# Optimization experiments

Measured on AMD Instinct MI355X. Metric: run time of the kernel, lower is better.

Reference implementation:

```python
import jax, jax.numpy as jnp
import numpy as np
from jax import lax

B, T, P, H, O = 64, 96, 256, 128, 24  # batch, seq_len, num_points, hidden_dim, pred_len


def setup_inputs() -> dict:
    key = jax.random.key(0)
    ks = jax.random.split(key, 7)
    s = 1.0 / np.sqrt(H)  # torch LSTM/Linear default init scale
    return {
        "x": jax.random.normal(ks[0], (B, T, P, 1), dtype=jnp.float32),
        "W_ih": jax.random.uniform(ks[1], (P, 4 * H, 1), jnp.float32, -s, s),
        "W_hh": jax.random.uniform(ks[2], (P, 4 * H, H), jnp.float32, -s, s),
        "b_ih": jax.random.uniform(ks[3], (P, 4 * H), jnp.float32, -s, s),
        "b_hh": jax.random.uniform(ks[4], (P, 4 * H), jnp.float32, -s, s),
        "W_fc": jax.random.uniform(ks[5], (P, O, H), jnp.float32, -s, s),
        "b_fc": jax.random.uniform(ks[6], (P, O), jnp.float32, -s, s),
    }


def reference(x, W_ih, W_hh, b_ih, b_hh, W_fc, b_fc):
    # x: [B, T, P, F]; model uses only feature 0
    xs = x[..., 0]  # [B, T, P]
    # input_dim == 1, so input-to-gate contribution is a scaled broadcast of W_ih
    # precompute for all timesteps: [T, B, P, 4H]
    gx = jnp.einsum("btp,pg->tbpg", xs, W_ih[:, :, 0]) + (b_ih + b_hh)

    def step(carry, gxt):
        h, c = carry  # [B, P, H] each
        gates = gxt + jnp.einsum("bph,pgh->bpg", h, W_hh)  # [B, P, 4H]
        i, f, g, o = jnp.split(gates, 4, axis=-1)  # torch gate order i,f,g,o
        i = jax.nn.sigmoid(i)
        f = jax.nn.sigmoid(f)
        g = jnp.tanh(g)
        o = jax.nn.sigmoid(o)
        c = f * c + i * g
        h = o * jnp.tanh(c)
        return (h, c), None

    h0 = jnp.zeros((B, P, H), dtype=x.dtype)
    (h, _), _ = lax.scan(step, (h0, h0), gx)
    # per-point Linear on final hidden state: [B, P, O]
    out = jnp.einsum("bph,poh->bpo", h, W_fc) + b_fc
    # original stacks point outputs on last dim -> [B, pred_len, P]
    return jnp.transpose(out, (0, 2, 1))
```

## Files before the change

### kernel.cpp

```cpp
#include <hip/hip_runtime.h>
#include <hip/hip_bf16.h>

#define Bdim 64
#define Tdim 96
#define Pdim 256
#define Hdim 128
#define Gdim 512
#define Odim 24
#define BH   32

typedef _Float16 f16x8 __attribute__((ext_vector_type(8)));
typedef float    f32x16 __attribute__((ext_vector_type(16)));
typedef float    f32x2  __attribute__((ext_vector_type(2)));

union H8 { uint4 u4; unsigned short s[8]; _Float16 h[8]; f16x8 v; };
union HS { _Float16 h; unsigned short s; };

__device__ __forceinline__ float exp2_fast(float x) {
#if __has_builtin(__builtin_amdgcn_exp2f)
    return __builtin_amdgcn_exp2f(x);
#else
    return __expf(x * 0.6931471805599453f);
#endif
}

__global__ __launch_bounds__(1024, 4)
void lstm_fused(const float* __restrict__ x,
                const float* __restrict__ W_ih,
                const float* __restrict__ W_hh,
                const float* __restrict__ b_ih,
                const float* __restrict__ b_hh,
                const float* __restrict__ W_fc,
                const float* __restrict__ b_fc,
                float* __restrict__ out)
{
    __shared__ unsigned short hb0[2][BH * Hdim];
    __shared__ unsigned short hb1[2][BH * Hdim];

    const int p   = blockIdx.x;
    const int tid = threadIdx.x;
    const int w   = tid >> 6;
    const int l31 = tid & 31;
    const int hi  = (tid >> 5) & 1;

    const float L1 = 1.4426950408889634f;
    const float L2 = 2.0f * L1;

    for (int i = tid; i < 2 * BH * Hdim; i += 1024) ((unsigned short*)hb0)[i] = 0;
    for (int i = tid; i < 2 * BH * Hdim; i += 1024) ((unsigned short*)hb1)[i] = 0;

    f16x8 afr[9];
    {
        const int rp   = w * 32 + l31;
        const int orow = ((rp & 3) << 7) | (rp >> 2);
        const float sc = ((rp & 3) == 2) ? L2 : L1;
        const float* rowp = W_hh + (size_t)p * Gdim * Hdim + (size_t)orow * Hdim;
        #pragma unroll
        for (int ks = 0; ks < 8; ++ks) {
            int k0 = ks * 16 + hi * 8;
            float4 va = *(const float4*)(rowp + k0);
            float4 vb = *(const float4*)(rowp + k0 + 4);
            H8 u;
            u.h[0] = (_Float16)(sc * va.x); u.h[1] = (_Float16)(sc * va.y);
            u.h[2] = (_Float16)(sc * va.z); u.h[3] = (_Float16)(sc * va.w);
            u.h[4] = (_Float16)(sc * vb.x); u.h[5] = (_Float16)(sc * vb.y);
            u.h[6] = (_Float16)(sc * vb.z); u.h[7] = (_Float16)(sc * vb.w);
            afr[ks] = u.v;
        }
        H8 u9;
        #pragma unroll
        for (int j = 0; j < 8; ++j) u9.s[j] = 0;
        if (hi == 0) {
            u9.h[0] = (_Float16)(sc * W_ih[(size_t)p * Gdim + orow]);
            u9.h[1] = (_Float16)(sc * (b_ih[(size_t)p * Gdim + orow] +
                                       b_hh[(size_t)p * Gdim + orow]));
        }
        afr[8] = u9.v;
    }

    auto ldh = [&](const unsigned short* hb, int ks) -> H8 {
        H8 r;
        int c   = ks * 2 + hi;
        int off = (l31 << 8) + ((c ^ (l31 & 15)) << 4);
        r.u4 = *(const uint4*)((const char*)hb + off);
        return r;
    };

    auto ep_pair = [&](const f32x16& a, int j, f32x2* cr, unsigned short* wb) {
        f32x2 yi = {a[8 * j + 0], a[8 * j + 4]};
        f32x2 yf = {a[8 * j + 1], a[8 * j + 5]};
        f32x2 yg = {a[8 * j + 2], a[8 * j + 6]};
        f32x2 yo = {a[8 * j + 3], a[8 * j + 7]};
        f32x2 Ef = {exp2_fast(-yf.x), exp2_fast(-yf.y)};
        f32x2 Ei = {exp2_fast(-yi.x), exp2_fast(-yi.y)};
        f32x2 Eg = {exp2_fast(yg.x),  exp2_fast(yg.y)};
        f32x2 t1 = Ef + 1.0f;
        f32x2 t2 = Ei + 1.0f;
        f32x2 t3 = Eg + 1.0f;
        f32x2 t4 = Eg - 1.0f;
        f32x2 den = (t1 * t2) * t3;
        f32x2 num = (cr[j] * t2) * t3 + (L2 * t4) * t1;
        float D = den.x * den.y;
        float r = __builtin_amdgcn_rcpf(D);
        f32x2 inv = {r * den.y, r * den.x};
        f32x2 cn  = num * inv;
        cn.x = __builtin_amdgcn_fmed3f(cn.x, -30.0f, 30.0f);
        cn.y = __builtin_amdgcn_fmed3f(cn.y, -30.0f, 30.0f);
        cr[j] = cn;
        f32x2 Eo = {exp2_fast(-yo.x), exp2_fast(-yo.y)};
        f32x2 Ec = {exp2_fast(cn.x),  exp2_fast(cn.y)};
        f32x2 d2 = (Eo + 1.0f) * (Ec + 1.0f);
        float D2 = d2.x * d2.y;
        float r2 = __builtin_amdgcn_rcpf(D2);
        f32x2 j2 = {r2 * d2.y, r2 * d2.x};
        f32x2 hv = (Ec - 1.0f) * j2;
        HS ha; ha.h = (_Float16)hv.x;
        HS hc; hc.h = (_Float16)hv.y;
        int base = (l31 << 7) + ((w ^ (l31 & 15)) << 3) + 4 * j + hi;
        wb[base]     = ha.s;
        wb[base + 2] = hc.s;
    };

    auto phase = [&](const unsigned short* rb, unsigned short* wb,
                     f32x16& acc, const f32x16& ar, f32x2* cr, float xv,
                     bool doGemm, bool doEp) {
        if (doGemm) {
            H8 f0 = ldh(rb, 0), f1 = ldh(rb, 1);
            H8 f2 = ldh(rb, 2), f3 = ldh(rb, 3);
            f32x16 z;
            #pragma unroll
            for (int j = 0; j < 16; ++j) z[j] = 0.f;
            acc = __builtin_amdgcn_mfma_f32_32x32x16_f16(afr[0], f0.v, z, 0, 0, 0);
            acc = __builtin_amdgcn_mfma_f32_32x32x16_f16(afr[1], f1.v, acc, 0, 0, 0);
            if (doEp) ep_pair(ar, 0, cr, wb);
            H8 f4 = ldh(rb, 4), f5 = ldh(rb, 5);
            acc = __builtin_amdgcn_mfma_f32_32x32x16_f16(afr[2], f2.v, acc, 0, 0, 0);
            acc = __builtin_amdgcn_mfma_f32_32x32x16_f16(afr[3], f3.v, acc, 0, 0, 0);
            if (doEp) ep_pair(ar, 1, cr, wb);
            H8 f6 = ldh(rb, 6), f7 = ldh(rb, 7);
            acc = __builtin_amdgcn_mfma_f32_32x32x16_f16(afr[4], f4.v, acc, 0, 0, 0);
            acc = __builtin_amdgcn_mfma_f32_32x32x16_f16(afr[5], f5.v, acc, 0, 0, 0);
            acc = __builtin_amdgcn_mfma_f32_32x32x16_f16(afr[6], f6.v, acc, 0, 0, 0);
            acc = __builtin_amdgcn_mfma_f32_32x32x16_f16(afr[7], f7.v, acc, 0, 0, 0);
            H8 bg;
            #pragma unroll
            for (int j = 0; j < 8; ++j) bg.s[j] = 0;
            if (hi == 0) { bg.h[0] = (_Float16)xv; bg.h[1] = (_Float16)1.0f; }
            acc = __builtin_amdgcn_mfma_f32_32x32x16_f16(afr[8], bg.v, acc, 0, 0, 0);
        } else if (doEp) {
            ep_pair(ar, 0, cr, wb);
            ep_pair(ar, 1, cr, wb);
        }
    };

    f32x2 cre0[2] = {f32x2{0.f, 0.f}, f32x2{0.f, 0.f}};
    f32x2 cre1[2] = {f32x2{0.f, 0.f}, f32x2{0.f, 0.f}};
    f32x16 acc0, acc1;
    #pragma unroll
    for (int j = 0; j < 16; ++j) { acc0[j] = 0.f; acc1[j] = 0.f; }

    const float* xp0 = x + (size_t)((0 * BH + l31) * Tdim) * Pdim + p;
    const float* xp1 = x + (size_t)((1 * BH + l31) * Tdim) * Pdim + p;
    float xv1 = xp1[0];

    __syncthreads();

    {
        float xv0 = xp0[0];
        phase(hb0[0], hb1[0], acc0, acc1, cre1, xv0, true, false);
    }
    __syncthreads();

    for (int t = 0; t < Tdim; ++t) {
        const int P  = t & 1;
        const int tn = (t + 1 < Tdim) ? (t + 1) : t;
        float xn0 = xp0[(size_t)tn * Pdim];

        phase(hb1[P], hb0[P ^ 1], acc1, acc0, cre0, xv1, true, true);
        __syncthreads();

        float xn1 = xp1[(size_t)tn * Pdim];
        if (t + 1 < Tdim) {
            phase(hb0[P ^ 1], hb1[P ^ 1], acc0, acc1, cre1, xn0, true, true);
        } else {
            phase(hb0[P ^ 1], hb1[P ^ 1], acc0, acc1, cre1, 0.f, false, true);
        }
        __syncthreads();
        xv1 = xn1;
    }

    const float* wfc = W_fc + (size_t)p * Odim * Hdim;
    const float* bfc = b_fc + (size_t)p * Odim;
    for (int i = tid; i < Bdim * Odim; i += 1024) {
        int o = i % Odim;
        int b = i / Odim;
        int bl = (b < BH) ? b : (b - BH);
        const unsigned short* hr = (b < BH) ? (hb0[0] + (bl << 7))
                                            : (hb1[0] + (bl << 7));
        float s = bfc[o];
        const float* wr = wfc + o * Hdim;
        #pragma unroll 8
        for (int k2 = 0; k2 < Hdim; ++k2) {
            int idx = (((k2 >> 3) ^ (bl & 15)) << 3) + (k2 & 7);
            HS s2; s2.s = hr[idx];
            s = __builtin_fmaf(wr[k2], (float)s2.h, s);
        }
        out[(size_t)b * Odim * Pdim + (size_t)o * Pdim + p] = s;
    }
}

extern "C" void kernel_launch(void* const* d_in, const int* in_sizes, int n_in,
                              void* d_out, int out_size, void* d_ws, size_t ws_size,
                              hipStream_t stream) {
    const float* x    = (const float*)d_in[0];
    const float* W_ih = (const float*)d_in[1];
    const float* W_hh = (const float*)d_in[2];
    const float* b_ih = (const float*)d_in[3];
    const float* b_hh = (const float*)d_in[4];
    const float* W_fc = (const float*)d_in[5];
    const float* b_fc = (const float*)d_in[6];
    float* out = (float*)d_out;

    lstm_fused<<<dim3(Pdim), dim3(1024), 0, stream>>>(x, W_ih, W_hh, b_ih, b_hh, W_fc, b_fc, out);
}
```

Before: 390.9 us.

## Split batch halves across separate blocks, each wave computing two gate tiles

Each point now gets two 512-thread blocks, one per batch half of 32, where before one 1024-thread block interleaved both halves in a software-pipelined ping-pong. Each wave holds two M-tiles of W_hh (16 fragments) and issues two interleaved MFMA chains that share the same h fragments. The bias/input term moves into a packed register, and hidden-state writes become packed 8-byte stores. This removes the two-phase interleaving and one barrier per step, and doubles the block count to fill more CUs, at the cost of loading W_hh twice per point and more VGPRs per thread.

```diff
diff --git a/kernel.cpp b/kernel.cpp
--- a/kernel.cpp
+++ b/kernel.cpp
@@ -9,12 +9,14 @@
 #define Odim 24
 #define BH   32
 
-typedef _Float16 f16x8 __attribute__((ext_vector_type(8)));
+typedef _Float16 f16x8  __attribute__((ext_vector_type(8)));
+typedef __fp16   fp16x2 __attribute__((ext_vector_type(2)));
 typedef float    f32x16 __attribute__((ext_vector_type(16)));
 typedef float    f32x2  __attribute__((ext_vector_type(2)));
 
-union H8 { uint4 u4; unsigned short s[8]; _Float16 h[8]; f16x8 v; };
+union H8 { uint4 u4; unsigned int u[4]; unsigned short s[8]; _Float16 h[8]; f16x8 v; };
 union HS { _Float16 h; unsigned short s; };
+union PK2 { fp16x2 v; unsigned int u; };
 
 __device__ __forceinline__ float exp2_fast(float x) {
 #if __has_builtin(__builtin_amdgcn_exp2f)
@@ -24,7 +26,9 @@
 #endif
 }
 
-__global__ __launch_bounds__(1024, 4)
+#define MFMA __builtin_amdgcn_mfma_f32_32x32x16_f16
+
+__global__ __launch_bounds__(512, 4)
 void lstm_fused(const float* __restrict__ x,
                 const float* __restrict__ W_ih,
                 const float* __restrict__ W_hh,
@@ -34,178 +38,169 @@
                 const float* __restrict__ b_fc,
                 float* __restrict__ out)
 {
-    __shared__ unsigned short hb0[2][BH * Hdim];
-    __shared__ unsigned short hb1[2][BH * Hdim];
-
-    const int p   = blockIdx.x;
-    const int tid = threadIdx.x;
-    const int w   = tid >> 6;
-    const int l31 = tid & 31;
-    const int hi  = (tid >> 5) & 1;
+    __shared__ unsigned short hbuf[2][BH * Hdim];
+
+    const int p    = blockIdx.x >> 1;
+    const int half = blockIdx.x & 1;
+    const int tid  = threadIdx.x;
+    const int w    = tid >> 6;
+    const int l31  = tid & 31;
+    const int hi   = (tid >> 5) & 1;
 
     const float L1 = 1.4426950408889634f;
     const float L2 = 2.0f * L1;
 
-    for (int i = tid; i < 2 * BH * Hdim; i += 1024) ((unsigned short*)hb0)[i] = 0;
-    for (int i = tid; i < 2 * BH * Hdim; i += 1024) ((unsigned short*)hb1)[i] = 0;
-
-    f16x8 afr[9];
+    for (int i = tid; i < 2 * BH * Hdim; i += 512) ((unsigned short*)hbuf)[i] = 0;
+
+    f16x8 afr[2][8];
+    unsigned int gxp[2];
     {
-        const int rp   = w * 32 + l31;
-        const int orow = ((rp & 3) << 7) | (rp >> 2);
-        const float sc = ((rp & 3) == 2) ? L2 : L1;
-        const float* rowp = W_hh + (size_t)p * Gdim * Hdim + (size_t)orow * Hdim;
+        const int gate = l31 & 3;
+        const float sc = (gate == 2) ? L2 : L1;
         #pragma unroll
-        for (int ks = 0; ks < 8; ++ks) {
-            int k0 = ks * 16 + hi * 8;
-            float4 va = *(const float4*)(rowp + k0);
-            float4 vb = *(const float4*)(rowp + k0 + 4);
-            H8 u;
-            u.h[0] = (_Float16)(sc * va.x); u.h[1] = (_Float16)(sc * va.y);
-            u.h[2] = (_Float16)(sc * va.z); u.h[3] = (_Float16)(sc * va.w);
-            u.h[4] = (_Float16)(sc * vb.x); u.h[5] = (_Float16)(sc * vb.y);
-            u.h[6] = (_Float16)(sc * vb.z); u.h[7] = (_Float16)(sc * vb.w);
-            afr[ks] = u.v;
-        }
-        H8 u9;
-        #pragma unroll
-        for (int j = 0; j < 8; ++j) u9.s[j] = 0;
-        if (hi == 0) {
-            u9.h[0] = (_Float16)(sc * W_ih[(size_t)p * Gdim + orow]);
-            u9.h[1] = (_Float16)(sc * (b_ih[(size_t)p * Gdim + orow] +
-                                       b_hh[(size_t)p * Gdim + orow]));
-        }
-        afr[8] = u9.v;
+        for (int m = 0; m < 2; ++m) {
+            const int kk   = 16 * w + 8 * m + 4 * ((l31 >> 2) & 1) + (l31 >> 3);
+            const int orow = gate * 128 + kk;
+            const float* rowp = W_hh + (size_t)p * Gdim * Hdim + (size_t)orow * Hdim;
+            #pragma unroll
+            for (int ks = 0; ks < 8; ++ks) {
+                int k0 = ks * 16 + hi * 8;
+                float4 va = *(const float4*)(rowp + k0);
+                float4 vb = *(const float4*)(rowp + k0 + 4);
+                H8 u;
+                u.h[0] = (_Float16)(sc * va.x); u.h[1] = (_Float16)(sc * va.y);
+                u.h[2] = (_Float16)(sc * va.z); u.h[3] = (_Float16)(sc * va.w);
+                u.h[4] = (_Float16)(sc * vb.x); u.h[5] = (_Float16)(sc * vb.y);
+                u.h[6] = (_Float16)(sc * vb.z); u.h[7] = (_Float16)(sc * vb.w);
+                afr[m][ks] = u.v;
+            }
+            HS ga, gb;
+            ga.h = (_Float16)(sc * W_ih[(size_t)p * Gdim + orow]);
+            gb.h = (_Float16)(sc * (b_ih[(size_t)p * Gdim + orow] +
+                                    b_hh[(size_t)p * Gdim + orow]));
+            gxp[m] = hi ? 0u : ((unsigned int)ga.s | ((unsigned int)gb.s << 16));
+        }
     }
 
-    auto ldh = [&](const unsigned short* hb, int ks) -> H8 {
-        H8 r;
-        int c   = ks * 2 + hi;
-        int off = (l31 << 8) + ((c ^ (l31 & 15)) << 4);
-        r.u4 = *(const uint4*)((const char*)hb + off);
-        return r;
-    };
-
-    auto ep_pair = [&](const f32x16& a, int j, f32x2* cr, unsigned short* wb) {
-        f32x2 yi = {a[8 * j + 0], a[8 * j + 4]};
-        f32x2 yf = {a[8 * j + 1], a[8 * j + 5]};
-        f32x2 yg = {a[8 * j + 2], a[8 * j + 6]};
-        f32x2 yo = {a[8 * j + 3], a[8 * j + 7]};
-        f32x2 Ef = {exp2_fast(-yf.x), exp2_fast(-yf.y)};
-        f32x2 Ei = {exp2_fast(-yi.x), exp2_fast(-yi.y)};
-        f32x2 Eg = {exp2_fast(yg.x),  exp2_fast(yg.y)};
-        f32x2 t1 = Ef + 1.0f;
-        f32x2 t2 = Ei + 1.0f;
-        f32x2 t3 = Eg + 1.0f;
-        f32x2 t4 = Eg - 1.0f;
-        f32x2 den = (t1 * t2) * t3;
-        f32x2 num = (cr[j] * t2) * t3 + (L2 * t4) * t1;
-        float D = den.x * den.y;
-        float r = __builtin_amdgcn_rcpf(D);
-        f32x2 inv = {r * den.y, r * den.x};
-        f32x2 cn  = num * inv;
-        cn.x = __builtin_amdgcn_fmed3f(cn.x, -30.0f, 30.0f);
-        cn.y = __builtin_amdgcn_fmed3f(cn.y, -30.0f, 30.0f);
-        cr[j] = cn;
-        f32x2 Eo = {exp2_fast(-yo.x), exp2_fast(-yo.y)};
-        f32x2 Ec = {exp2_fast(cn.x),  exp2_fast(cn.y)};
-        f32x2 d2 = (Eo + 1.0f) * (Ec + 1.0f);
-        float D2 = d2.x * d2.y;
-        float r2 = __builtin_amdgcn_rcpf(D2);
-        f32x2 j2 = {r2 * d2.y, r2 * d2.x};
-        f32x2 hv = (Ec - 1.0f) * j2;
-        HS ha; ha.h = (_Float16)hv.x;
-        HS hc; hc.h = (_Float16)hv.y;
-        int base = (l31 << 7) + ((w ^ (l31 & 15)) << 3) + 4 * j + hi;
-        wb[base]     = ha.s;
-        wb[base + 2] = hc.s;
-    };
-
-    auto phase = [&](const unsigned short* rb, unsigned short* wb,
-                     f32x16& acc, const f32x16& ar, f32x2* cr, float xv,
-                     bool doGemm, bool doEp) {
-        if (doGemm) {
-            H8 f0 = ldh(rb, 0), f1 = ldh(rb, 1);
-            H8 f2 = ldh(rb, 2), f3 = ldh(rb, 3);
+    const int rb0 = (l31 << 8) | ((hi ^ (l31 & 15)) << 4);
+    const int wo0 = (l31 << 8) + (((2 * w + 0) ^ (l31 & 15)) << 4) + (hi << 3);
+    const int wo1 = (l31 << 8) + (((2 * w + 1) ^ (l31 & 15)) << 4) + (hi << 3);
+
+    f32x2 cre[4];
+    #pragma unroll
+    for (int i = 0; i < 4; ++i) cre[i] = f32x2{0.f, 0.f};
+
+    const float* xp = x + (size_t)((half * BH + l31) * Tdim) * Pdim + p;
+    float xv = xp[0];
+
+    __syncthreads();
+
+    for (int t = 0; t < Tdim; ++t) {
+        const unsigned short* rbuf = hbuf[t & 1];
+        unsigned short* wbuf = hbuf[(t & 1) ^ 1];
+        const char* rc = (const char*)rbuf;
+        float xn = xp[(size_t)((t + 1 < Tdim) ? t + 1 : t) * Pdim];
+
+        PK2 xb; xb.v = __builtin_amdgcn_cvt_pkrtz(xv, 1.0f);
+        H8 bg; bg.u[0] = hi ? 0u : xb.u; bg.u[1] = 0; bg.u[2] = 0; bg.u[3] = 0;
+        H8 g0; g0.u[0] = gxp[0]; g0.u[1] = 0; g0.u[2] = 0; g0.u[3] = 0;
+        H8 g1; g1.u[0] = gxp[1]; g1.u[1] = 0; g1.u[2] = 0; g1.u[3] = 0;
+
+        f32x16 acc0, acc1;
+        {
+            H8 f0, f1, f2, f3, f4, f5, f6, f7;
+            f0.u4 = *(const uint4*)(rc + (rb0 ^ (0 << 5)));
+            f1.u4 = *(const uint4*)(rc + (rb0 ^ (1 << 5)));
+            f2.u4 = *(const uint4*)(rc + (rb0 ^ (2 << 5)));
+            f3.u4 = *(const uint4*)(rc + (rb0 ^ (3 << 5)));
             f32x16 z;
             #pragma unroll
             for (int j = 0; j < 16; ++j) z[j] = 0.f;
-            acc = __builtin_amdgcn_mfma_f32_32x32x16_f16(afr[0], f0.v, z, 0, 0, 0);
-            acc = __builtin_amdgcn_mfma_f32_32x32x16_f16(afr[1], f1.v, acc, 0, 0, 0);
-            if (doEp) ep_pair(ar, 0, cr, wb);
-            H8 f4 = ldh(rb, 4), f5 = ldh(rb, 5);
-            acc = __builtin_amdgcn_mfma_f32_32x32x16_f16(afr[2], f2.v, acc, 0, 0, 0);
-            acc = __builtin_amdgcn_mfma_f32_32x32x16_f16(afr[3], f3.v, acc, 0, 0, 0);
-            if (doEp) ep_pair(ar, 1, cr, wb);
-            H8 f6 = ldh(rb, 6), f7 = ldh(rb, 7);
-            acc = __builtin_amdgcn_mfma_f32_32x32x16_f16(afr[4], f4.v, acc, 0, 0, 0);
-            acc = __builtin_amdgcn_mfma_f32_32x32x16_f16(afr[5], f5.v, acc, 0, 0, 0);
-            acc = __builtin_amdgcn_mfma_f32_32x32x16_f16(afr[6], f6.v, acc, 0, 0, 0);
-            acc = __builtin_amdgcn_mfma_f32_32x32x16_f16(afr[7], f7.v, acc, 0, 0, 0);
-            H8 bg;
+            acc0 = MFMA(afr[0][0], f0.v, z, 0, 0, 0);
+            acc1 = MFMA(afr[1][0], f0.v, z, 0, 0, 0);
+            f4.u4 = *(const uint4*)(rc + (rb0 ^ (4 << 5)));
+            acc0 = MFMA(afr[0][1], f1.v, acc0, 0, 0, 0);
+            acc1 = MFMA(afr[1][1], f1.v, acc1, 0, 0, 0);
+            f5.u4 = *(const uint4*)(rc + (rb0 ^ (5 << 5)));
+            acc0 = MFMA(afr[0][2], f2.v, acc0, 0, 0, 0);
+            acc1 = MFMA(afr[1][2], f2.v, acc1, 0, 0, 0);
+            f6.u4 = *(const uint4*)(rc + (rb0 ^ (6 << 5)));
+            acc0 = MFMA(afr[0][3], f3.v, acc0, 0, 0, 0);
+            acc1 = MFMA(afr[1][3], f3.v, acc1, 0, 0, 0);
+            f7.u4 = *(const uint4*)(rc + (rb0 ^ (7 << 5)));
+            acc0 = MFMA(afr[0][4], f4.v, acc0, 0, 0, 0);
+            acc1 = MFMA(afr[1][4], f4.v, acc1, 0, 0, 0);
+            acc0 = MFMA(afr[0][5], f5.v, acc0, 0, 0, 0);
+            acc1 = MFMA(afr[1][5], f5.v, acc1, 0, 0, 0);
+            acc0 = MFMA(afr[0][6], f6.v, acc0, 0, 0, 0);
+            acc1 = MFMA(afr[1][6], f6.v, acc1, 0, 0, 0);
+            acc0 = MFMA(afr[0][7], f7.v, acc0, 0, 0, 0);
+            acc1 = MFMA(afr[1][7], f7.v, acc1, 0, 0, 0);
+            acc0 = MFMA(g0.v, bg.v, acc0, 0, 0, 0);
+            acc1 = MFMA(g1.v, bg.v, acc1, 0, 0, 0);
+        }
+
+        #pragma unroll
+        for (int m = 0; m < 2; ++m) {
+            const f32x16& a = m ? acc1 : acc0;
+            f32x2 hv[2];
             #pragma unroll
-            for (int j = 0; j < 8; ++j) bg.s[j] = 0;
-            if (hi == 0) { bg.h[0] = (_Float16)xv; bg.h[1] = (_Float16)1.0f; }
-            acc = __builtin_amdgcn_mfma_f32_32x32x16_f16(afr[8], bg.v, acc, 0, 0, 0);
-        } else if (doEp) {
-            ep_pair(ar, 0, cr, wb);
-            ep_pair(ar, 1, cr, wb);
-        }
-    };
-
-    f32x2 cre0[2] = {f32x2{0.f, 0.f}, f32x2{0.f, 0.f}};
-    f32x2 cre1[2] = {f32x2{0.f, 0.f}, f32x2{0.f, 0.f}};
-    f32x16 acc0, acc1;
-    #pragma unroll
-    for (int j = 0; j < 16; ++j) { acc0[j] = 0.f; acc1[j] = 0.f; }
-
-    const float* xp0 = x + (size_t)((0 * BH + l31) * Tdim) * Pdim + p;
-    const float* xp1 = x + (size_t)((1 * BH + l31) * Tdim) * Pdim + p;
-    float xv1 = xp1[0];
-
-    __syncthreads();
-
-    {
-        float xv0 = xp0[0];
-        phase(hb0[0], hb1[0], acc0, acc1, cre1, xv0, true, false);
-    }
-    __syncthreads();
-
-    for (int t = 0; t < Tdim; ++t) {
-        const int P  = t & 1;
-        const int tn = (t + 1 < Tdim) ? (t + 1) : t;
-        float xn0 = xp0[(size_t)tn * Pdim];
-
-        phase(hb1[P], hb0[P ^ 1], acc1, acc0, cre0, xv1, true, true);
+            for (int j = 0; j < 2; ++j) {
+                f32x2 yi = {a[8 * j + 0], a[8 * j + 4]};
+                f32x2 yf = {a[8 * j + 1], a[8 * j + 5]};
+                f32x2 yg = {a[8 * j + 2], a[8 * j + 6]};
+                f32x2 yo = {a[8 * j + 3], a[8 * j + 7]};
+                f32x2 Ef = {exp2_fast(-yf.x), exp2_fast(-yf.y)};
+                f32x2 Ei = {exp2_fast(-yi.x), exp2_fast(-yi.y)};
+                f32x2 Eg = {exp2_fast(yg.x),  exp2_fast(yg.y)};
+                f32x2 t1 = Ef + 1.0f;
+                f32x2 t2 = Ei + 1.0f;
+                f32x2 t3 = Eg + 1.0f;
+                f32x2 t4 = Eg - 1.0f;
+                f32x2 den = (t1 * t2) * t3;
+                f32x2 num = (cre[m * 2 + j] * t2) * t3 + (L2 * t4) * t1;
+                float D = den.x * den.y;
+                float r = __builtin_amdgcn_rcpf(D);
+                f32x2 inv = {r * den.y, r * den.x};
+                f32x2 cn  = num * inv;
+                cn.x = __builtin_amdgcn_fmed3f(cn.x, -30.0f, 30.0f);
+                cn.y = __builtin_amdgcn_fmed3f(cn.y, -30.0f, 30.0f);
+                cre[m * 2 + j] = cn;
+                f32x2 Eo = {exp2_fast(-yo.x), exp2_fast(-yo.y)};
+                f32x2 Ec = {exp2_fast(cn.x),  exp2_fast(cn.y)};
+                f32x2 d2 = (Eo + 1.0f) * (Ec + 1.0f);
+                float D2 = d2.x * d2.y;
+                float r2 = __builtin_amdgcn_rcpf(D2);
+                f32x2 j2 = {r2 * d2.y, r2 * d2.x};
+                hv[j] = (Ec - 1.0f) * j2;
+            }
+            PK2 lo, hi2;
+            lo.v  = __builtin_amdgcn_cvt_pkrtz(hv[0].x, hv[0].y);
+            hi2.v = __builtin_amdgcn_cvt_pkrtz(hv[1].x, hv[1].y);
+            uint2 valw = {lo.u, hi2.u};
+            *(uint2*)((char*)wbuf + (m ? wo1 : wo0)) = valw;
+        }
+
         __syncthreads();
-
-        float xn1 = xp1[(size_t)tn * Pdim];
-        if (t + 1 < Tdim) {
-            phase(hb0[P ^ 1], hb1[P ^ 1], acc0, acc1, cre1, xn0, true, true);
-        } else {
-            phase(hb0[P ^ 1], hb1[P ^ 1], acc0, acc1, cre1, 0.f, false, true);
-        }
-        __syncthreads();
-        xv1 = xn1;
+        xv = xn;
     }
 
     const float* wfc = W_fc + (size_t)p * Odim * Hdim;
     const float* bfc = b_fc + (size_t)p * Odim;
-    for (int i = tid; i < Bdim * Odim; i += 1024) {
+    for (int i = tid; i < BH * Odim; i += 512) {
         int o = i % Odim;
         int b = i / Odim;
-        int bl = (b < BH) ? b : (b - BH);
-        const unsigned short* hr = (b < BH) ? (hb0[0] + (bl << 7))
-                                            : (hb1[0] + (bl << 7));
+        const unsigned short* hr = hbuf[0] + (b << 7);
         float s = bfc[o];
         const float* wr = wfc + o * Hdim;
         #pragma unroll 8
         for (int k2 = 0; k2 < Hdim; ++k2) {
-            int idx = (((k2 >> 3) ^ (bl & 15)) << 3) + (k2 & 7);
+            int idx = (((k2 >> 3) ^ (b & 15)) << 3) + (k2 & 7);
             HS s2; s2.s = hr[idx];
             s = __builtin_fmaf(wr[k2], (float)s2.h, s);
         }
-        out[(size_t)b * Odim * Pdim + (size_t)o * Pdim + p] = s;
+        int bg2 = half * BH + b;
+        out[(size_t)bg2 * Odim * Pdim + (size_t)o * Pdim + p] = s;
     }
 }
 
@@ -221,5 +216,5 @@
     const float* b_fc = (const float*)d_in[6];
     float* out = (float*)d_out;
 
-    lstm_fused<<<dim3(Pdim), dim3(1024), 0, stream>>>(x, W_ih, W_hh, b_ih, b_hh, W_fc, b_fc, out);
+    lstm_fused<<<dim3(2 * Pdim), dim3(512), 0, stream>>>(x, W_ih, W_hh, b_ih, b_hh, W_fc, b_fc, out);
 }
```

After: 418.8 us. 7.1% more time.
